# Kernel tuning notes

Hardware: AMD Instinct MI355X
Metric: run time of the kernel (lower is better)

Reference implementation:

```python
import jax, jax.numpy as jnp
import numpy as np
import math

HIDDEN = 768
NUM_HEADS = 12
HEAD_DIM = HIDDEN // NUM_HEADS
EPS = 1e-05
MU_LEARNED = 0.0    # registered buffer init value (inference mode)
SIGMA_LEARNED = 1.0 # registered buffer init value (inference mode)
SCALES = (0.5, 1.0, 2.0)


def make_pe(n, d):
    # Sinusoidal positional encoding, identical to PositionalEncoding buffer.
    pos = np.arange(n, dtype=np.float32)[:, None]
    div = np.exp(np.arange(0, d, 2, dtype=np.float32) * (-math.log(10000.0) / d))
    pe = np.zeros((n, d), dtype=np.float32)
    pe[:, 0::2] = np.sin(pos * div)
    pe[:, 1::2] = np.cos(pos * div)
    return jnp.asarray(pe)


def setup_inputs() -> dict:
    key = jax.random.key(0)
    ks = jax.random.split(key, 12)
    B, C, Hh, Ww = 8, 256, 32, 32
    feat = jax.random.normal(ks[0], (B, C, Hh, Ww), jnp.float32)
    I = jax.random.uniform(ks[1], (B, 1, Hh, Ww), jnp.float32)
    sc_c = 1.0 / math.sqrt(C)
    sd = 1.0 / math.sqrt(HIDDEN)
    proj_w = jax.random.normal(ks[2], (C, HIDDEN), jnp.float32) * sc_c  # 1x1 conv as matmul
    proj_b = jnp.zeros((HIDDEN,), jnp.float32)
    wq = jax.random.normal(ks[3], (HIDDEN, HIDDEN), jnp.float32) * sd
    bq = jnp.zeros((HIDDEN,), jnp.float32)
    wk = jax.random.normal(ks[4], (HIDDEN, HIDDEN), jnp.float32) * sd
    bk = jnp.zeros((HIDDEN,), jnp.float32)
    wv = jax.random.normal(ks[5], (HIDDEN, HIDDEN), jnp.float32) * sd
    bv = jnp.zeros((HIDDEN,), jnp.float32)
    wo = jax.random.normal(ks[6], (HIDDEN, HIDDEN), jnp.float32) * sd
    bo = jnp.zeros((HIDDEN,), jnp.float32)
    lam = jnp.float32(0.5)
    return dict(feat=feat, I=I, proj_w=proj_w, proj_b=proj_b,
                wq=wq, bq=bq, wk=wk, bk=bk, wv=wv, bv=bv, wo=wo, bo=bo, lam=lam)


def reference(feat, I, proj_w, proj_b, wq, bq, wk, bk, wv, bv, wo, bo, lam):
    B, C, Hh, Ww = feat.shape
    N = Hh * Ww
    # HiddenFeatureProjection: 1x1 conv projection -> flatten -> tokens [B, N, D]
    tokens = jnp.einsum('bchw,cd->bhwd', feat, proj_w).reshape(B, N, HIDDEN) + proj_b
    tokens = tokens + make_pe(N, HIDDEN)[None]
    # GaussianWeightModule (inference path, learned buffers mu=0, sigma=1)
    G = sum(jnp.exp(-(I - MU_LEARNED) ** 2 / (2.0 * (k * SIGMA_LEARNED) ** 2 + EPS))
            for k in SCALES) / float(len(SCALES))  # [B,1,H,W]
    g = G.reshape(B, N)                              # H*W == N by construction
    bias = g[:, :, None] * g[:, None, :]             # [B, N, N] outer product
    # GaussianEnhancedAttention
    q = (tokens @ wq + bq).reshape(B, N, NUM_HEADS, HEAD_DIM).transpose(0, 2, 1, 3)
    k = (tokens @ wk + bk).reshape(B, N, NUM_HEADS, HEAD_DIM).transpose(0, 2, 1, 3)
    v = (tokens @ wv + bv).reshape(B, N, NUM_HEADS, HEAD_DIM).transpose(0, 2, 1, 3)
    scores = jnp.einsum('bhnd,bhmd->bhnm', q, k) / math.sqrt(HEAD_DIM)
    scores = scores + lam * bias[:, None, :, :]
    attn = jax.nn.softmax(scores, axis=-1)
    out = jnp.einsum('bhnm,bhmd->bhnd', attn, v).transpose(0, 2, 1, 3).reshape(B, N, HIDDEN)
    return out @ wo + bo
```

## Files before the change

### kernel.cpp

```cpp
#include <hip/hip_runtime.h>
#include <hip/hip_bf16.h>
#include <math.h>

#define HIDDEN 768
#define NHEADS 12
#define HDIM   64
#define NTOK   1024
#define BATCH  8
#define CIN    256
#define M_ALL  (BATCH * NTOK)
#define LSTR   72

typedef __hip_bfloat16 bf16;
typedef short frag8 __attribute__((ext_vector_type(8)));
typedef float f32x4 __attribute__((ext_vector_type(4)));

#define GL2LDS(gp, lp) \
    __builtin_amdgcn_global_load_lds((const __attribute__((address_space(1))) void*)(gp), \
                                     (__attribute__((address_space(3))) void*)(lp), 16, 0, 0)

__device__ __forceinline__ short f2bs(float x){
    union { bf16 h; short s; } u; u.h = __float2bfloat16(x); return u.s;
}

__device__ __forceinline__ float gaussw(float x){
    float x2 = x * x;
    return (__expf(-x2 / 0.50001f) + __expf(-x2 / 2.00001f) + __expf(-x2 / 8.00001f)) * (1.0f / 3.0f);
}

__global__ __launch_bounds__(256) void prep_all(
    const float* __restrict__ wq, const float* __restrict__ wk,
    const float* __restrict__ wv, const float* __restrict__ wo,
    const float* __restrict__ proj_w, const float* __restrict__ feat,
    short* __restrict__ wtqkv, short* __restrict__ wtp, short* __restrict__ featT)
{
    __shared__ short t[64][65];
    const int blk = blockIdx.x;
    const float* W; short* WT; int K, N, k0, n0;
    if (blk < 576) {
        int p = blk / 144, rem = blk % 144;
        const float* srcs[4] = {wq, wk, wv, wo};
        W = srcs[p]; WT = wtqkv + (size_t)p * HIDDEN * HIDDEN;
        K = HIDDEN; N = HIDDEN; k0 = (rem / 12) * 64; n0 = (rem % 12) * 64;
    } else if (blk < 624) {
        int rem = blk - 576;
        W = proj_w; WT = wtp;
        K = CIN; N = HIDDEN; k0 = (rem / 12) * 64; n0 = (rem % 12) * 64;
    } else {
        int rem = blk - 624;
        int b = rem / 64; rem %= 64;
        W = feat + (size_t)b * CIN * NTOK; WT = featT + (size_t)b * NTOK * CIN;
        K = CIN; N = NTOK; k0 = (rem / 16) * 64; n0 = (rem % 16) * 64;
    }
    const int tid = threadIdx.x;
    #pragma unroll
    for (int it = 0; it < 16; it++) {
        int e = tid + 256 * it;
        int kk = e / 64, nn = e % 64;
        t[kk][nn] = f2bs(W[(size_t)(k0 + kk) * N + n0 + nn]);
    }
    __syncthreads();
    #pragma unroll
    for (int it = 0; it < 16; it++) {
        int e = tid + 256 * it;
        int nn = e / 64, kk = e % 64;
        WT[(size_t)(n0 + nn) * K + k0 + kk] = t[kk][nn];
    }
}

__global__ __launch_bounds__(256) void transpose_v(
    const short* __restrict__ v, short* __restrict__ vT)
{
    __shared__ short t[64][65];
    const int nt = blockIdx.x;
    const int bh = blockIdx.y;
    const int b = bh / NHEADS, h = bh % NHEADS;
    const int tid = threadIdx.x;
    #pragma unroll
    for (int it = 0; it < 16; it++) {
        int e = tid + 256 * it;
        int rr = e / 64, cc = e % 64;
        t[rr][cc] = v[(size_t)(b * NTOK + nt * 64 + rr) * HIDDEN + h * HDIM + cc];
    }
    __syncthreads();
    #pragma unroll
    for (int it = 0; it < 16; it++) {
        int e = tid + 256 * it;
        int c2 = e / 64, r2 = e % 64;
        vT[((size_t)bh * HDIM + c2) * NTOK + nt * 64 + r2] = t[r2][c2];
    }
}

__global__ __launch_bounds__(256) void gemm_mfma128(
    const short* __restrict__ A, const short* __restrict__ WT0, long wt_z,
    const float* __restrict__ b0, const float* __restrict__ b1, const float* __restrict__ b2,
    short* o0, short* o1, short* o2, int K)
{
    __shared__ short Al[128 * 32];
    __shared__ short Bl[128 * 32];
    const int z = blockIdx.z;
    const short* WT  = WT0 + (size_t)z * wt_z;
    const float* bias = (z == 0) ? b0 : (z == 1) ? b1 : b2;
    short* outv       = (z == 0) ? o0 : (z == 1) ? o1 : o2;

    const int tid  = threadIdx.x;
    const int m0   = blockIdx.x * 128;
    const int n0   = blockIdx.y * 128;
    const int lane = tid & 63, wid = tid >> 6;
    const int wm   = (wid >> 1) * 64, wn = (wid & 1) * 64;
    const int l16  = lane & 15, quad = lane >> 4;

    const int sr  = lane >> 2;
    const int ssg = (lane & 3) ^ ((sr >> 1) & 3);
    const int fsw = (l16 >> 1) & 3;

    const f32x4 z4 = {0.f, 0.f, 0.f, 0.f};
    f32x4 acc[4][4];
    #pragma unroll
    for (int i = 0; i < 4; i++)
        #pragma unroll
        for (int j = 0; j < 4; j++) acc[i][j] = z4;

    for (int k0 = 0; k0 < K; k0 += 32) {
        #pragma unroll
        for (int t = 0; t < 2; t++) {
            int rbase = wid * 32 + t * 16;
            int r = rbase + sr;
            GL2LDS(A  + (size_t)(m0 + r) * K + k0 + ssg * 8, &Al[rbase * 32]);
            GL2LDS(WT + (size_t)(n0 + r) * K + k0 + ssg * 8, &Bl[rbase * 32]);
        }
        __syncthreads();
        frag8 af[4], bfr[4];
        #pragma unroll
        for (int i = 0; i < 4; i++)
            af[i]  = *(const frag8*)&Al[(wm + i * 16 + l16) * 32 + ((quad ^ fsw) * 8)];
        #pragma unroll
        for (int j = 0; j < 4; j++)
            bfr[j] = *(const frag8*)&Bl[(wn + j * 16 + l16) * 32 + ((quad ^ fsw) * 8)];
        #pragma unroll
        for (int i = 0; i < 4; i++)
            #pragma unroll
            for (int j = 0; j < 4; j++)
                acc[i][j] = __builtin_amdgcn_mfma_f32_16x16x32_bf16(af[i], bfr[j], acc[i][j], 0, 0, 0);
        __syncthreads();
    }

    #pragma unroll
    for (int i = 0; i < 4; i++) {
        #pragma unroll
        for (int r = 0; r < 4; r++) {
            int m = m0 + wm + i * 16 + quad * 4 + r;
            #pragma unroll
            for (int j = 0; j < 4; j++) {
                int col = n0 + wn + j * 16 + l16;
                outv[(size_t)m * HIDDEN + col] = f2bs(acc[i][j][r] + bias[col]);
            }
        }
    }
}

template<int MODE>
__global__ __launch_bounds__(256) void gemm_mfma64(
    const short* __restrict__ A, const short* __restrict__ WT,
    const float* __restrict__ bias, void* outv, int K)
{
    __shared__ short Al[64 * 32];
    __shared__ short Bl[128 * 32];
    const int tid  = threadIdx.x;
    const int m0   = blockIdx.x * 64;
    const int n0   = blockIdx.y * 128;
    const int lane = tid & 63, wid = tid >> 6;
    const int wn   = wid * 32;
    const int l16  = lane & 15, quad = lane >> 4;

    const int sr  = lane >> 2;
    const int ssg = (lane & 3) ^ ((sr >> 1) & 3);
    const int fsw = (l16 >> 1) & 3;

    const f32x4 z4 = {0.f, 0.f, 0.f, 0.f};
    f32x4 acc[4][2];
    #pragma unroll
    for (int i = 0; i < 4; i++)
        #pragma unroll
        for (int j = 0; j < 2; j++) acc[i][j] = z4;

    for (int k0 = 0; k0 < K; k0 += 32) {
        GL2LDS(A + (size_t)(m0 + wid * 16 + sr) * K + k0 + ssg * 8, &Al[(wid * 16) * 32]);
        #pragma unroll
        for (int t = 0; t < 2; t++) {
            int rbase = wid * 32 + t * 16;
            GL2LDS(WT + (size_t)(n0 + rbase + sr) * K + k0 + ssg * 8, &Bl[rbase * 32]);
        }
        __syncthreads();
        frag8 af[4], bfr[2];
        #pragma unroll
        for (int i = 0; i < 4; i++)
            af[i]  = *(const frag8*)&Al[(i * 16 + l16) * 32 + ((quad ^ fsw) * 8)];
        #pragma unroll
        for (int j = 0; j < 2; j++)
            bfr[j] = *(const frag8*)&Bl[(wn + j * 16 + l16) * 32 + ((quad ^ fsw) * 8)];
        #pragma unroll
        for (int i = 0; i < 4; i++)
            #pragma unroll
            for (int j = 0; j < 2; j++)
                acc[i][j] = __builtin_amdgcn_mfma_f32_16x16x32_bf16(af[i], bfr[j], acc[i][j], 0, 0, 0);
        __syncthreads();
    }

    const float kfac = -9.210340371976184f / 768.0f;
    #pragma unroll
    for (int i = 0; i < 4; i++) {
        #pragma unroll
        for (int r = 0; r < 4; r++) {
            int m = m0 + i * 16 + quad * 4 + r;
            #pragma unroll
            for (int j = 0; j < 2; j++) {
                int col = n0 + wn + j * 16 + l16;
                float val = acc[i][j][r] + bias[col];
                if (MODE == 1) {
                    int n_tok = m & (NTOK - 1);
                    float ang = (float)n_tok * expf((float)(2 * (col >> 1)) * kfac);
                    val += (col & 1) ? cosf(ang) : sinf(ang);
                }
                if (MODE == 2) ((float*)outv)[(size_t)m * HIDDEN + col] = val;
                else           ((short*)outv)[(size_t)m * HIDDEN + col] = f2bs(val);
            }
        }
    }
}

__global__ __launch_bounds__(256, 3) void attn_mfma(
    const short* __restrict__ q, const short* __restrict__ k, const short* __restrict__ vT,
    const float* __restrict__ I, const float* __restrict__ lam_p, short* __restrict__ out)
{
    __shared__ short QP[128 * LSTR];
    __shared__ short Ks[64 * 64];
    __shared__ short Vt[64 * 64];
    __shared__ float gL[NTOK];

    const int tid  = threadIdx.x;
    const int lin  = blockIdx.x;
    const int xcd  = lin & 7, slot = lin >> 3;
    const int b    = xcd;
    const int h    = slot >> 3;
    const int qt   = slot & 7;
    const float L2E  = 1.4426950408889634f;
    const float lam2 = lam_p[0] * L2E;
    const float scl  = 0.125f * L2E;
    const int lane = tid & 63, wave = tid >> 6;
    const int l16  = lane & 15, quad = lane >> 4;

    const int sr   = lane >> 3;
    const int slin = lane & 7;
    const int ssg  = slin ^ sr;
    const int fsw  = l16 & 7;

    for (int i = tid; i < NTOK; i += 256) gL[i] = gaussw(I[b * NTOK + i]);

    #pragma unroll
    for (int it = 0; it < 4; it++) {
        int e = tid + 256 * it;
        int r = e >> 3, seg = e & 7;
        *(frag8*)&QP[r * LSTR + seg * 8] =
            *(const frag8*)&q[(size_t)(b * NTOK + qt * 128 + r) * HIDDEN + h * HDIM + seg * 8];
    }
    __syncthreads();

    frag8 aq[2][2];
    #pragma unroll
    for (int half = 0; half < 2; half++) {
        aq[half][0] = *(const frag8*)&QP[(wave * 32 + half * 16 + l16) * LSTR + quad * 8];
        aq[half][1] = *(const frag8*)&QP[(wave * 32 + half * 16 + l16) * LSTR + 32 + quad * 8];
    }
    float gi[2][4];
    #pragma unroll
    for (int half = 0; half < 2; half++)
        #pragma unroll
        for (int r = 0; r < 4; r++)
            gi[half][r] = gL[qt * 128 + wave * 32 + half * 16 + quad * 4 + r];

    const f32x4 z4 = {0.f, 0.f, 0.f, 0.f};
    f32x4 o_acc[2][4];
    #pragma unroll
    for (int half = 0; half < 2; half++)
        #pragma unroll
        for (int d = 0; d < 4; d++) o_acc[half][d] = z4;
    float l_run[2][4] = {};

    const size_t kb  = (size_t)b * NTOK * HIDDEN + h * HDIM;
    const size_t vtb = (size_t)(b * NHEADS + h) * HDIM * NTOK;

    for (int jt = 0; jt < 16; jt++) {
        __syncthreads();
        #pragma unroll
        for (int t = 0; t < 2; t++) {
            int rbase = wave * 16 + t * 8;
            int r = rbase + sr;
            GL2LDS(k  + kb  + (size_t)(jt * 64 + r) * HIDDEN + ssg * 8, &Ks[rbase * 64]);
            GL2LDS(vT + vtb + (size_t)r * NTOK + jt * 64 + ssg * 8,     &Vt[rbase * 64]);
        }
        __syncthreads();

        float p[2][4][4];
        #pragma unroll
        for (int t4 = 0; t4 < 4; t4++) {
            frag8 bk0 = *(const frag8*)&Ks[(t4 * 16 + l16) * 64 + ((quad ^ fsw) * 8)];
            frag8 bk1 = *(const frag8*)&Ks[(t4 * 16 + l16) * 64 + (((quad + 4) ^ fsw) * 8)];
            #pragma unroll
            for (int half = 0; half < 2; half++) {
                f32x4 a = z4;
                a = __builtin_amdgcn_mfma_f32_16x16x32_bf16(aq[half][0], bk0, a, 0, 0, 0);
                a = __builtin_amdgcn_mfma_f32_16x16x32_bf16(aq[half][1], bk1, a, 0, 0, 0);
                #pragma unroll
                for (int r = 0; r < 4; r++) p[half][t4][r] = a[r];
            }
        }

        float gjs[4];
        #pragma unroll
        for (int t4 = 0; t4 < 4; t4++) gjs[t4] = lam2 * gL[jt * 64 + t4 * 16 + l16];

        #pragma unroll
        for (int half = 0; half < 2; half++)
            #pragma unroll
            for (int t4 = 0; t4 < 4; t4++)
                #pragma unroll
                for (int r = 0; r < 4; r++) {
                    float e = exp2f(p[half][t4][r] * scl + gi[half][r] * gjs[t4]);
                    l_run[half][r] += e;
                    QP[(wave * 32 + half * 16 + quad * 4 + r) * LSTR + t4 * 16 + l16] = f2bs(e);
                }

        frag8 ap[2][2];
        #pragma unroll
        for (int half = 0; half < 2; half++) {
            ap[half][0] = *(const frag8*)&QP[(wave * 32 + half * 16 + l16) * LSTR + quad * 8];
            ap[half][1] = *(const frag8*)&QP[(wave * 32 + half * 16 + l16) * LSTR + 32 + quad * 8];
        }
        #pragma unroll
        for (int d = 0; d < 4; d++) {
            frag8 bv0 = *(const frag8*)&Vt[(d * 16 + l16) * 64 + ((quad ^ fsw) * 8)];
            frag8 bv1 = *(const frag8*)&Vt[(d * 16 + l16) * 64 + (((quad + 4) ^ fsw) * 8)];
            #pragma unroll
            for (int half = 0; half < 2; half++) {
                o_acc[half][d] = __builtin_amdgcn_mfma_f32_16x16x32_bf16(ap[half][0], bv0, o_acc[half][d], 0, 0, 0);
                o_acc[half][d] = __builtin_amdgcn_mfma_f32_16x16x32_bf16(ap[half][1], bv1, o_acc[half][d], 0, 0, 0);
            }
        }
    }

    #pragma unroll
    for (int half = 0; half < 2; half++)
        #pragma unroll
        for (int r = 0; r < 4; r++) {
            float l = l_run[half][r];
            #pragma unroll
            for (int off = 1; off < 16; off <<= 1) l += __shfl_xor(l, off);
            float inv_l = 1.0f / l;
            int row = qt * 128 + wave * 32 + half * 16 + quad * 4 + r;
            #pragma unroll
            for (int d = 0; d < 4; d++)
                out[(size_t)(b * NTOK + row) * HIDDEN + h * HDIM + d * 16 + l16]
                    = f2bs(o_acc[half][d][r] * inv_l);
        }
}

extern "C" void kernel_launch(void* const* d_in, const int* in_sizes, int n_in,
                              void* d_out, int out_size, void* d_ws, size_t ws_size,
                              hipStream_t stream)
{
    const float* feat   = (const float*)d_in[0];
    const float* I      = (const float*)d_in[1];
    const float* proj_w = (const float*)d_in[2];
    const float* proj_b = (const float*)d_in[3];
    const float* wq     = (const float*)d_in[4];
    const float* bq     = (const float*)d_in[5];
    const float* wk     = (const float*)d_in[6];
    const float* bk     = (const float*)d_in[7];
    const float* wv     = (const float*)d_in[8];
    const float* bv     = (const float*)d_in[9];
    const float* wo     = (const float*)d_in[10];
    const float* bo     = (const float*)d_in[11];
    const float* lam    = (const float*)d_in[12];
    float* out = (float*)d_out;

    short* wtqkv = (short*)d_ws;
    short* wto   = wtqkv + (size_t)3 * HIDDEN * HIDDEN;
    short* wtp   = wto   + (size_t)HIDDEN * HIDDEN;
    short* tokens= wtp   + (size_t)HIDDEN * CIN;
    short* qbuf  = tokens+ (size_t)M_ALL * HIDDEN;
    short* featT = qbuf;
    short* vTb   = tokens;
    short* kbuf  = (short*)d_out;
    short* vbuf  = kbuf + (size_t)M_ALL * HIDDEN;

    prep_all<<<1136, 256, 0, stream>>>(wq, wk, wv, wo, proj_w, feat, wtqkv, wtp, featT);
    gemm_mfma64<1><<<dim3(128, 6), 256, 0, stream>>>(featT, wtp, proj_b, tokens, CIN);
    gemm_mfma128<<<dim3(64, 6, 3), 256, 0, stream>>>(tokens, wtqkv, (long)HIDDEN * HIDDEN,
                                                     bq, bk, bv,
                                                     qbuf, kbuf, vbuf, HIDDEN);
    transpose_v<<<dim3(16, 96), 256, 0, stream>>>(vbuf, vTb);
    attn_mfma<<<768, 256, 0, stream>>>(qbuf, kbuf, vTb, I, lam, qbuf);
    gemm_mfma64<2><<<dim3(128, 6), 256, 0, stream>>>(qbuf, wto, bo, out, HIDDEN);
}
```

Before: 241.7 us.

## Fold input projection into QKV weights to shrink the QKV GEMM reduction

Precomposes proj_w with Wq/Wk/Wv, and precomputes (PE + proj_b)·W + b per token position, using two small GEMMs. The QKV GEMM then runs directly on the transposed input features with K=256 instead of K=768, and the separate token-projection GEMM is removed. The positional and bias term is added in the epilogue from a bf16 table. In exchange there are extra small GEMMs and extra bf16 rounding of the composed weights and the bias table, which may slightly change accuracy.

```diff
diff --git a/kernel.cpp b/kernel.cpp
--- a/kernel.cpp
+++ b/kernel.cpp
@@ -22,6 +22,9 @@
 __device__ __forceinline__ short f2bs(float x){
     union { bf16 h; short s; } u; u.h = __float2bfloat16(x); return u.s;
 }
+__device__ __forceinline__ float bs2f(short s){
+    union { short s; bf16 h; } u; u.s = s; return __bfloat162float(u.h);
+}
 
 __device__ __forceinline__ float gaussw(float x){
     float x2 = x * x;
@@ -31,40 +34,59 @@
 __global__ __launch_bounds__(256) void prep_all(
     const float* __restrict__ wq, const float* __restrict__ wk,
     const float* __restrict__ wv, const float* __restrict__ wo,
-    const float* __restrict__ proj_w, const float* __restrict__ feat,
-    short* __restrict__ wtqkv, short* __restrict__ wtp, short* __restrict__ featT)
-{
-    __shared__ short t[64][65];
+    const float* __restrict__ proj_w, const float* __restrict__ proj_b,
+    const float* __restrict__ feat,
+    short* __restrict__ wtqkv, short* __restrict__ wpc,
+    short* __restrict__ featT, short* __restrict__ PEb)
+{
     const int blk = blockIdx.x;
-    const float* W; short* WT; int K, N, k0, n0;
-    if (blk < 576) {
-        int p = blk / 144, rem = blk % 144;
-        const float* srcs[4] = {wq, wk, wv, wo};
-        W = srcs[p]; WT = wtqkv + (size_t)p * HIDDEN * HIDDEN;
-        K = HIDDEN; N = HIDDEN; k0 = (rem / 12) * 64; n0 = (rem % 12) * 64;
-    } else if (blk < 624) {
-        int rem = blk - 576;
-        W = proj_w; WT = wtp;
-        K = CIN; N = HIDDEN; k0 = (rem / 12) * 64; n0 = (rem % 12) * 64;
+    const int tid = threadIdx.x;
+
+    if (blk < 576 || (blk >= 588 && blk < 1100)) {
+        __shared__ short t[64][65];
+        const float* W; short* WT; int K, N, k0, n0;
+        if (blk < 576) {
+            int p = blk / 144, rem = blk % 144;
+            const float* srcs[4] = {wq, wk, wv, wo};
+            W = srcs[p]; WT = wtqkv + (size_t)p * HIDDEN * HIDDEN;
+            K = HIDDEN; N = HIDDEN; k0 = (rem / 12) * 64; n0 = (rem % 12) * 64;
+        } else {
+            int rem = blk - 588;
+            int b = rem / 64; rem %= 64;
+            W = feat + (size_t)b * CIN * NTOK; WT = featT + (size_t)b * NTOK * CIN;
+            K = CIN; N = NTOK; k0 = (rem / 16) * 64; n0 = (rem % 16) * 64;
+        }
+        #pragma unroll
+        for (int it = 0; it < 16; it++) {
+            int e = tid + 256 * it;
+            int kk = e / 64, nn = e % 64;
+            t[kk][nn] = f2bs(W[(size_t)(k0 + kk) * N + n0 + nn]);
+        }
+        __syncthreads();
+        #pragma unroll
+        for (int it = 0; it < 16; it++) {
+            int e = tid + 256 * it;
+            int nn = e / 64, kk = e % 64;
+            WT[(size_t)(n0 + nn) * K + k0 + kk] = t[kk][nn];
+        }
+    } else if (blk < 588) {
+        int base = (blk - 576) * 16384;
+        #pragma unroll
+        for (int it = 0; it < 64; it++) {
+            int e = base + it * 256 + tid;
+            wpc[e] = f2bs(proj_w[e]);
+        }
     } else {
-        int rem = blk - 624;
-        int b = rem / 64; rem %= 64;
-        W = feat + (size_t)b * CIN * NTOK; WT = featT + (size_t)b * NTOK * CIN;
-        K = CIN; N = NTOK; k0 = (rem / 16) * 64; n0 = (rem % 16) * 64;
-    }
-    const int tid = threadIdx.x;
-    #pragma unroll
-    for (int it = 0; it < 16; it++) {
-        int e = tid + 256 * it;
-        int kk = e / 64, nn = e % 64;
-        t[kk][nn] = f2bs(W[(size_t)(k0 + kk) * N + n0 + nn]);
-    }
-    __syncthreads();
-    #pragma unroll
-    for (int it = 0; it < 16; it++) {
-        int e = tid + 256 * it;
-        int nn = e / 64, kk = e % 64;
-        WT[(size_t)(n0 + nn) * K + k0 + kk] = t[kk][nn];
+        const float kfac = -9.210340371976184f / 768.0f;
+        int n0 = (blk - 1100) * 64;
+        for (int it = 0; it < 192; it++) {
+            int e = it * 256 + tid;
+            int r = e / HIDDEN, d = e % HIDDEN;
+            int n = n0 + r;
+            float ang = (float)n * __expf((float)(2 * (d >> 1)) * kfac);
+            float pe  = (d & 1) ? __cosf(ang) : __sinf(ang);
+            PEb[(size_t)n * HIDDEN + d] = f2bs(pe + proj_b[d]);
+        }
     }
 }
 
@@ -91,17 +113,20 @@
     }
 }
 
-__global__ __launch_bounds__(256) void gemm_mfma128(
-    const short* __restrict__ A, const short* __restrict__ WT0, long wt_z,
+__global__ __launch_bounds__(256) void gemm_pre(
+    const short* __restrict__ Abase, long a_z,
+    const short* __restrict__ WTbase, long wt_z,
+    short* __restrict__ obase, long o_z, int ldo,
     const float* __restrict__ b0, const float* __restrict__ b1, const float* __restrict__ b2,
-    short* o0, short* o1, short* o2, int K)
+    int K)
 {
     __shared__ short Al[128 * 32];
     __shared__ short Bl[128 * 32];
     const int z = blockIdx.z;
-    const short* WT  = WT0 + (size_t)z * wt_z;
+    const short* A  = Abase  + (size_t)z * a_z;
+    const short* WT = WTbase + (size_t)z * wt_z;
+    short* outv     = obase  + (size_t)z * o_z;
     const float* bias = (z == 0) ? b0 : (z == 1) ? b1 : b2;
-    short* outv       = (z == 0) ? o0 : (z == 1) ? o1 : o2;
 
     const int tid  = threadIdx.x;
     const int m0   = blockIdx.x * 128;
@@ -153,16 +178,87 @@
             #pragma unroll
             for (int j = 0; j < 4; j++) {
                 int col = n0 + wn + j * 16 + l16;
-                outv[(size_t)m * HIDDEN + col] = f2bs(acc[i][j][r] + bias[col]);
+                float val = acc[i][j][r];
+                if (bias) val += bias[col];
+                outv[(size_t)m * ldo + col] = f2bs(val);
             }
         }
     }
 }
 
-template<int MODE>
-__global__ __launch_bounds__(256) void gemm_mfma64(
+__global__ __launch_bounds__(256) void gemm_qkv(
+    const short* __restrict__ A, const short* __restrict__ WcT,
+    const short* __restrict__ CpeB,
+    short* o0, short* o1, short* o2)
+{
+    __shared__ short Al[128 * 32];
+    __shared__ short Bl[128 * 32];
+    const int z = blockIdx.z;
+    const short* WT  = WcT  + (size_t)z * HIDDEN * CIN;
+    const short* Cpe = CpeB + (size_t)z * NTOK * HIDDEN;
+    short* outv      = (z == 0) ? o0 : (z == 1) ? o1 : o2;
+
+    const int tid  = threadIdx.x;
+    const int m0   = blockIdx.x * 128;
+    const int n0   = blockIdx.y * 128;
+    const int lane = tid & 63, wid = tid >> 6;
+    const int wm   = (wid >> 1) * 64, wn = (wid & 1) * 64;
+    const int l16  = lane & 15, quad = lane >> 4;
+
+    const int sr  = lane >> 2;
+    const int ssg = (lane & 3) ^ ((sr >> 1) & 3);
+    const int fsw = (l16 >> 1) & 3;
+
+    const f32x4 z4 = {0.f, 0.f, 0.f, 0.f};
+    f32x4 acc[4][4];
+    #pragma unroll
+    for (int i = 0; i < 4; i++)
+        #pragma unroll
+        for (int j = 0; j < 4; j++) acc[i][j] = z4;
+
+    for (int k0 = 0; k0 < CIN; k0 += 32) {
+        #pragma unroll
+        for (int t = 0; t < 2; t++) {
+            int rbase = wid * 32 + t * 16;
+            int r = rbase + sr;
+            GL2LDS(A  + (size_t)(m0 + r) * CIN + k0 + ssg * 8, &Al[rbase * 32]);
+            GL2LDS(WT + (size_t)(n0 + r) * CIN + k0 + ssg * 8, &Bl[rbase * 32]);
+        }
+        __syncthreads();
+        frag8 af[4], bfr[4];
+        #pragma unroll
+        for (int i = 0; i < 4; i++)
+            af[i]  = *(const frag8*)&Al[(wm + i * 16 + l16) * 32 + ((quad ^ fsw) * 8)];
+        #pragma unroll
+        for (int j = 0; j < 4; j++)
+            bfr[j] = *(const frag8*)&Bl[(wn + j * 16 + l16) * 32 + ((quad ^ fsw) * 8)];
+        #pragma unroll
+        for (int i = 0; i < 4; i++)
+            #pragma unroll
+            for (int j = 0; j < 4; j++)
+                acc[i][j] = __builtin_amdgcn_mfma_f32_16x16x32_bf16(af[i], bfr[j], acc[i][j], 0, 0, 0);
+        __syncthreads();
+    }
+
+    #pragma unroll
+    for (int i = 0; i < 4; i++) {
+        #pragma unroll
+        for (int r = 0; r < 4; r++) {
+            int m = m0 + wm + i * 16 + quad * 4 + r;
+            int nt = m & (NTOK - 1);
+            #pragma unroll
+            for (int j = 0; j < 4; j++) {
+                int col = n0 + wn + j * 16 + l16;
+                outv[(size_t)m * HIDDEN + col] =
+                    f2bs(acc[i][j][r] + bs2f(Cpe[(size_t)nt * HIDDEN + col]));
+            }
+        }
+    }
+}
+
+__global__ __launch_bounds__(256) void gemm_final(
     const short* __restrict__ A, const short* __restrict__ WT,
-    const float* __restrict__ bias, void* outv, int K)
+    const float* __restrict__ bias, float* __restrict__ outv, int K)
 {
     __shared__ short Al[64 * 32];
     __shared__ short Bl[128 * 32];
@@ -207,7 +303,6 @@
         __syncthreads();
     }
 
-    const float kfac = -9.210340371976184f / 768.0f;
     #pragma unroll
     for (int i = 0; i < 4; i++) {
         #pragma unroll
@@ -216,14 +311,7 @@
             #pragma unroll
             for (int j = 0; j < 2; j++) {
                 int col = n0 + wn + j * 16 + l16;
-                float val = acc[i][j][r] + bias[col];
-                if (MODE == 1) {
-                    int n_tok = m & (NTOK - 1);
-                    float ang = (float)n_tok * expf((float)(2 * (col >> 1)) * kfac);
-                    val += (col & 1) ? cosf(ang) : sinf(ang);
-                }
-                if (MODE == 2) ((float*)outv)[(size_t)m * HIDDEN + col] = val;
-                else           ((short*)outv)[(size_t)m * HIDDEN + col] = f2bs(val);
+                outv[(size_t)m * HIDDEN + col] = acc[i][j][r] + bias[col];
             }
         }
     }
@@ -386,20 +474,29 @@
 
     short* wtqkv = (short*)d_ws;
     short* wto   = wtqkv + (size_t)3 * HIDDEN * HIDDEN;
-    short* wtp   = wto   + (size_t)HIDDEN * HIDDEN;
-    short* tokens= wtp   + (size_t)HIDDEN * CIN;
-    short* qbuf  = tokens+ (size_t)M_ALL * HIDDEN;
-    short* featT = qbuf;
-    short* vTb   = tokens;
+    short* reg2  = wtqkv + (size_t)4 * HIDDEN * HIDDEN;
+    short* wpc   = reg2;
+    short* PEb   = wpc  + (size_t)CIN * HIDDEN;
+    short* featT = PEb  + (size_t)NTOK * HIDDEN;
+    short* WcT   = featT + (size_t)M_ALL * CIN;
+    short* CpeB  = WcT  + (size_t)3 * HIDDEN * CIN;
+    short* vTb   = reg2;
+    short* qbuf  = reg2 + (size_t)M_ALL * HIDDEN;
     short* kbuf  = (short*)d_out;
     short* vbuf  = kbuf + (size_t)M_ALL * HIDDEN;
 
-    prep_all<<<1136, 256, 0, stream>>>(wq, wk, wv, wo, proj_w, feat, wtqkv, wtp, featT);
-    gemm_mfma64<1><<<dim3(128, 6), 256, 0, stream>>>(featT, wtp, proj_b, tokens, CIN);
-    gemm_mfma128<<<dim3(64, 6, 3), 256, 0, stream>>>(tokens, wtqkv, (long)HIDDEN * HIDDEN,
-                                                     bq, bk, bv,
-                                                     qbuf, kbuf, vbuf, HIDDEN);
+    prep_all<<<1116, 256, 0, stream>>>(wq, wk, wv, wo, proj_w, proj_b, feat,
+                                       wtqkv, wpc, featT, PEb);
+    gemm_pre<<<dim3(6, 2, 3), 256, 0, stream>>>(wtqkv, (long)HIDDEN * HIDDEN,
+                                                wpc, 0,
+                                                WcT, (long)HIDDEN * CIN, CIN,
+                                                nullptr, nullptr, nullptr, HIDDEN);
+    gemm_pre<<<dim3(8, 6, 3), 256, 0, stream>>>(PEb, 0,
+                                                wtqkv, (long)HIDDEN * HIDDEN,
+                                                CpeB, (long)NTOK * HIDDEN, HIDDEN,
+                                                bq, bk, bv, HIDDEN);
+    gemm_qkv<<<dim3(64, 6, 3), 256, 0, stream>>>(featT, WcT, CpeB, qbuf, kbuf, vbuf);
     transpose_v<<<dim3(16, 96), 256, 0, stream>>>(vbuf, vTb);
     attn_mfma<<<768, 256, 0, stream>>>(qbuf, kbuf, vTb, I, lam, qbuf);
-    gemm_mfma64<2><<<dim3(128, 6), 256, 0, stream>>>(qbuf, wto, bo, out, HIDDEN);
-}
+    gemm_final<<<dim3(128, 6), 256, 0, stream>>>(qbuf, wto, bo, out, HIDDEN);
+}
```

Measured after the change: 278.5 us. 15.2% more time.

## Fuse V transpose into QKV GEMM epilogue and halve attention query tile

Applied to the files above, without the earlier changes.

The QKV GEMM now writes V directly in transposed per-head layout. It stages the tile through enlarged shared memory, which removes the separate transpose_v kernel and its extra global round trip. The attention kernel now processes 64 query rows per block instead of 128, doubling the grid to 1536 blocks and dropping the occupancy hint. This buys more parallelism and lower register pressure, but each K/V tile is now reused by fewer queries, so K/V traffic doubles.

```diff
diff --git a/kernel.cpp b/kernel.cpp
--- a/kernel.cpp
+++ b/kernel.cpp
@@ -68,40 +68,17 @@
     }
 }
 
-__global__ __launch_bounds__(256) void transpose_v(
-    const short* __restrict__ v, short* __restrict__ vT)
-{
-    __shared__ short t[64][65];
-    const int nt = blockIdx.x;
-    const int bh = blockIdx.y;
-    const int b = bh / NHEADS, h = bh % NHEADS;
-    const int tid = threadIdx.x;
-    #pragma unroll
-    for (int it = 0; it < 16; it++) {
-        int e = tid + 256 * it;
-        int rr = e / 64, cc = e % 64;
-        t[rr][cc] = v[(size_t)(b * NTOK + nt * 64 + rr) * HIDDEN + h * HDIM + cc];
-    }
-    __syncthreads();
-    #pragma unroll
-    for (int it = 0; it < 16; it++) {
-        int e = tid + 256 * it;
-        int c2 = e / 64, r2 = e % 64;
-        vT[((size_t)bh * HDIM + c2) * NTOK + nt * 64 + r2] = t[r2][c2];
-    }
-}
-
-__global__ __launch_bounds__(256) void gemm_mfma128(
+__global__ __launch_bounds__(256) void gemm_qkv(
     const short* __restrict__ A, const short* __restrict__ WT0, long wt_z,
     const float* __restrict__ b0, const float* __restrict__ b1, const float* __restrict__ b2,
-    short* o0, short* o1, short* o2, int K)
-{
-    __shared__ short Al[128 * 32];
-    __shared__ short Bl[128 * 32];
+    short* o0, short* o1, short* vT, int K)
+{
+    __shared__ short pool[128 * 136];
+    short* Al = pool;
+    short* Bl = pool + 128 * 32;
     const int z = blockIdx.z;
     const short* WT  = WT0 + (size_t)z * wt_z;
     const float* bias = (z == 0) ? b0 : (z == 1) ? b1 : b2;
-    short* outv       = (z == 0) ? o0 : (z == 1) ? o1 : o2;
 
     const int tid  = threadIdx.x;
     const int m0   = blockIdx.x * 128;
@@ -145,16 +122,42 @@
         __syncthreads();
     }
 
-    #pragma unroll
-    for (int i = 0; i < 4; i++) {
-        #pragma unroll
-        for (int r = 0; r < 4; r++) {
-            int m = m0 + wm + i * 16 + quad * 4 + r;
-            #pragma unroll
-            for (int j = 0; j < 4; j++) {
-                int col = n0 + wn + j * 16 + l16;
-                outv[(size_t)m * HIDDEN + col] = f2bs(acc[i][j][r] + bias[col]);
+    if (z != 2) {
+        short* outv = (z == 0) ? o0 : o1;
+        #pragma unroll
+        for (int i = 0; i < 4; i++)
+            #pragma unroll
+            for (int r = 0; r < 4; r++) {
+                int m = m0 + wm + i * 16 + quad * 4 + r;
+                #pragma unroll
+                for (int j = 0; j < 4; j++) {
+                    int col = n0 + wn + j * 16 + l16;
+                    outv[(size_t)m * HIDDEN + col] = f2bs(acc[i][j][r] + bias[col]);
+                }
             }
+    } else {
+        #pragma unroll
+        for (int i = 0; i < 4; i++)
+            #pragma unroll
+            for (int r = 0; r < 4; r++) {
+                int mloc = wm + i * 16 + quad * 4 + r;
+                #pragma unroll
+                for (int j = 0; j < 4; j++) {
+                    int cc = wn + j * 16 + l16;
+                    pool[cc * 136 + mloc] = f2bs(acc[i][j][r] + bias[n0 + cc]);
+                }
+            }
+        __syncthreads();
+        const int bb   = m0 >> 10;
+        const int nloc = m0 & 1023;
+        #pragma unroll
+        for (int it = 0; it < 8; it++) {
+            int cc  = (tid >> 4) + it * 16;
+            int seg = tid & 15;
+            int gcol = n0 + cc;
+            short* dst = vT + ((size_t)(bb * NHEADS + (gcol >> 6)) * HDIM + (gcol & 63)) * NTOK
+                            + nloc + seg * 8;
+            *(frag8*)dst = *(const frag8*)&pool[cc * 136 + seg * 8];
         }
     }
 }
@@ -229,11 +232,11 @@
     }
 }
 
-__global__ __launch_bounds__(256, 3) void attn_mfma(
+__global__ __launch_bounds__(256) void attn_mfma(
     const short* __restrict__ q, const short* __restrict__ k, const short* __restrict__ vT,
     const float* __restrict__ I, const float* __restrict__ lam_p, short* __restrict__ out)
 {
-    __shared__ short QP[128 * LSTR];
+    __shared__ short QP[64 * LSTR];
     __shared__ short Ks[64 * 64];
     __shared__ short Vt[64 * 64];
     __shared__ float gL[NTOK];
@@ -242,8 +245,8 @@
     const int lin  = blockIdx.x;
     const int xcd  = lin & 7, slot = lin >> 3;
     const int b    = xcd;
-    const int h    = slot >> 3;
-    const int qt   = slot & 7;
+    const int h    = slot >> 4;
+    const int qt   = slot & 15;
     const float L2E  = 1.4426950408889634f;
     const float lam2 = lam_p[0] * L2E;
     const float scl  = 0.125f * L2E;
@@ -258,34 +261,25 @@
     for (int i = tid; i < NTOK; i += 256) gL[i] = gaussw(I[b * NTOK + i]);
 
     #pragma unroll
-    for (int it = 0; it < 4; it++) {
+    for (int it = 0; it < 2; it++) {
         int e = tid + 256 * it;
         int r = e >> 3, seg = e & 7;
         *(frag8*)&QP[r * LSTR + seg * 8] =
-            *(const frag8*)&q[(size_t)(b * NTOK + qt * 128 + r) * HIDDEN + h * HDIM + seg * 8];
+            *(const frag8*)&q[(size_t)(b * NTOK + qt * 64 + r) * HIDDEN + h * HDIM + seg * 8];
     }
     __syncthreads();
 
-    frag8 aq[2][2];
-    #pragma unroll
-    for (int half = 0; half < 2; half++) {
-        aq[half][0] = *(const frag8*)&QP[(wave * 32 + half * 16 + l16) * LSTR + quad * 8];
-        aq[half][1] = *(const frag8*)&QP[(wave * 32 + half * 16 + l16) * LSTR + 32 + quad * 8];
-    }
-    float gi[2][4];
-    #pragma unroll
-    for (int half = 0; half < 2; half++)
-        #pragma unroll
-        for (int r = 0; r < 4; r++)
-            gi[half][r] = gL[qt * 128 + wave * 32 + half * 16 + quad * 4 + r];
+    frag8 aq0 = *(const frag8*)&QP[(wave * 16 + l16) * LSTR + quad * 8];
+    frag8 aq1 = *(const frag8*)&QP[(wave * 16 + l16) * LSTR + 32 + quad * 8];
+    float gi[4];
+    #pragma unroll
+    for (int r = 0; r < 4; r++) gi[r] = gL[qt * 64 + wave * 16 + quad * 4 + r];
 
     const f32x4 z4 = {0.f, 0.f, 0.f, 0.f};
-    f32x4 o_acc[2][4];
-    #pragma unroll
-    for (int half = 0; half < 2; half++)
-        #pragma unroll
-        for (int d = 0; d < 4; d++) o_acc[half][d] = z4;
-    float l_run[2][4] = {};
+    f32x4 o_acc[4];
+    #pragma unroll
+    for (int d = 0; d < 4; d++) o_acc[d] = z4;
+    float l_run[4] = {};
 
     const size_t kb  = (size_t)b * NTOK * HIDDEN + h * HDIM;
     const size_t vtb = (size_t)(b * NHEADS + h) * HDIM * NTOK;
@@ -301,68 +295,54 @@
         }
         __syncthreads();
 
-        float p[2][4][4];
+        float p[4][4];
         #pragma unroll
         for (int t4 = 0; t4 < 4; t4++) {
             frag8 bk0 = *(const frag8*)&Ks[(t4 * 16 + l16) * 64 + ((quad ^ fsw) * 8)];
             frag8 bk1 = *(const frag8*)&Ks[(t4 * 16 + l16) * 64 + (((quad + 4) ^ fsw) * 8)];
-            #pragma unroll
-            for (int half = 0; half < 2; half++) {
-                f32x4 a = z4;
-                a = __builtin_amdgcn_mfma_f32_16x16x32_bf16(aq[half][0], bk0, a, 0, 0, 0);
-                a = __builtin_amdgcn_mfma_f32_16x16x32_bf16(aq[half][1], bk1, a, 0, 0, 0);
-                #pragma unroll
-                for (int r = 0; r < 4; r++) p[half][t4][r] = a[r];
+            f32x4 a = z4;
+            a = __builtin_amdgcn_mfma_f32_16x16x32_bf16(aq0, bk0, a, 0, 0, 0);
+            a = __builtin_amdgcn_mfma_f32_16x16x32_bf16(aq1, bk1, a, 0, 0, 0);
+            #pragma unroll
+            for (int r = 0; r < 4; r++) p[t4][r] = a[r];
+        }
+
+        float gjs[4];
+        #pragma unroll
+        for (int t4 = 0; t4 < 4; t4++) gjs[t4] = lam2 * gL[jt * 64 + t4 * 16 + l16];
+
+        #pragma unroll
+        for (int t4 = 0; t4 < 4; t4++)
+            #pragma unroll
+            for (int r = 0; r < 4; r++) {
+                float e = exp2f(p[t4][r] * scl + gi[r] * gjs[t4]);
+                l_run[r] += e;
+                QP[(wave * 16 + quad * 4 + r) * LSTR + t4 * 16 + l16] = f2bs(e);
             }
-        }
-
-        float gjs[4];
-        #pragma unroll
-        for (int t4 = 0; t4 < 4; t4++) gjs[t4] = lam2 * gL[jt * 64 + t4 * 16 + l16];
-
-        #pragma unroll
-        for (int half = 0; half < 2; half++)
-            #pragma unroll
-            for (int t4 = 0; t4 < 4; t4++)
-                #pragma unroll
-                for (int r = 0; r < 4; r++) {
-                    float e = exp2f(p[half][t4][r] * scl + gi[half][r] * gjs[t4]);
-                    l_run[half][r] += e;
-                    QP[(wave * 32 + half * 16 + quad * 4 + r) * LSTR + t4 * 16 + l16] = f2bs(e);
-                }
-
-        frag8 ap[2][2];
-        #pragma unroll
-        for (int half = 0; half < 2; half++) {
-            ap[half][0] = *(const frag8*)&QP[(wave * 32 + half * 16 + l16) * LSTR + quad * 8];
-            ap[half][1] = *(const frag8*)&QP[(wave * 32 + half * 16 + l16) * LSTR + 32 + quad * 8];
-        }
+
+        frag8 ap0 = *(const frag8*)&QP[(wave * 16 + l16) * LSTR + quad * 8];
+        frag8 ap1 = *(const frag8*)&QP[(wave * 16 + l16) * LSTR + 32 + quad * 8];
         #pragma unroll
         for (int d = 0; d < 4; d++) {
             frag8 bv0 = *(const frag8*)&Vt[(d * 16 + l16) * 64 + ((quad ^ fsw) * 8)];
             frag8 bv1 = *(const frag8*)&Vt[(d * 16 + l16) * 64 + (((quad + 4) ^ fsw) * 8)];
-            #pragma unroll
-            for (int half = 0; half < 2; half++) {
-                o_acc[half][d] = __builtin_amdgcn_mfma_f32_16x16x32_bf16(ap[half][0], bv0, o_acc[half][d], 0, 0, 0);
-                o_acc[half][d] = __builtin_amdgcn_mfma_f32_16x16x32_bf16(ap[half][1], bv1, o_acc[half][d], 0, 0, 0);
-            }
-        }
-    }
-
-    #pragma unroll
-    for (int half = 0; half < 2; half++)
-        #pragma unroll
-        for (int r = 0; r < 4; r++) {
-            float l = l_run[half][r];
-            #pragma unroll
-            for (int off = 1; off < 16; off <<= 1) l += __shfl_xor(l, off);
-            float inv_l = 1.0f / l;
-            int row = qt * 128 + wave * 32 + half * 16 + quad * 4 + r;
-            #pragma unroll
-            for (int d = 0; d < 4; d++)
-                out[(size_t)(b * NTOK + row) * HIDDEN + h * HDIM + d * 16 + l16]
-                    = f2bs(o_acc[half][d][r] * inv_l);
-        }
+            o_acc[d] = __builtin_amdgcn_mfma_f32_16x16x32_bf16(ap0, bv0, o_acc[d], 0, 0, 0);
+            o_acc[d] = __builtin_amdgcn_mfma_f32_16x16x32_bf16(ap1, bv1, o_acc[d], 0, 0, 0);
+        }
+    }
+
+    #pragma unroll
+    for (int r = 0; r < 4; r++) {
+        float l = l_run[r];
+        #pragma unroll
+        for (int off = 1; off < 16; off <<= 1) l += __shfl_xor(l, off);
+        float inv_l = 1.0f / l;
+        int row = qt * 64 + wave * 16 + quad * 4 + r;
+        #pragma unroll
+        for (int d = 0; d < 4; d++)
+            out[(size_t)(b * NTOK + row) * HIDDEN + h * HDIM + d * 16 + l16]
+                = f2bs(o_acc[d][r] * inv_l);
+    }
 }
 
 extern "C" void kernel_launch(void* const* d_in, const int* in_sizes, int n_in,
@@ -386,20 +366,18 @@
 
     short* wtqkv = (short*)d_ws;
     short* wto   = wtqkv + (size_t)3 * HIDDEN * HIDDEN;
-    short* wtp   = wto   + (size_t)HIDDEN * HIDDEN;
+    short* wtp   = wtqkv + (size_t)4 * HIDDEN * HIDDEN;
     short* tokens= wtp   + (size_t)HIDDEN * CIN;
     short* qbuf  = tokens+ (size_t)M_ALL * HIDDEN;
     short* featT = qbuf;
-    short* vTb   = tokens;
     short* kbuf  = (short*)d_out;
-    short* vbuf  = kbuf + (size_t)M_ALL * HIDDEN;
+    short* vTb   = kbuf + (size_t)M_ALL * HIDDEN;
 
     prep_all<<<1136, 256, 0, stream>>>(wq, wk, wv, wo, proj_w, feat, wtqkv, wtp, featT);
     gemm_mfma64<1><<<dim3(128, 6), 256, 0, stream>>>(featT, wtp, proj_b, tokens, CIN);
-    gemm_mfma128<<<dim3(64, 6, 3), 256, 0, stream>>>(tokens, wtqkv, (long)HIDDEN * HIDDEN,
-                                                     bq, bk, bv,
-                                                     qbuf, kbuf, vbuf, HIDDEN);
-    transpose_v<<<dim3(16, 96), 256, 0, stream>>>(vbuf, vTb);
-    attn_mfma<<<768, 256, 0, stream>>>(qbuf, kbuf, vTb, I, lam, qbuf);
+    gemm_qkv<<<dim3(64, 6, 3), 256, 0, stream>>>(tokens, wtqkv, (long)HIDDEN * HIDDEN,
+                                                 bq, bk, bv,
+                                                 qbuf, kbuf, vTb, HIDDEN);
+    attn_mfma<<<1536, 256, 0, stream>>>(qbuf, kbuf, vTb, I, lam, qbuf);
     gemm_mfma64<2><<<dim3(128, 6), 256, 0, stream>>>(qbuf, wto, bo, out, HIDDEN);
 }
```

After: 246.9 us. +2.2%, slower.
